# Kernel optimization log

Hardware: AMD Instinct MI355X
Metric: run time of the kernel (lower is better)

The kernel has to match this reference:

```python
import jax, jax.numpy as jnp
import numpy as np

SLOPE = 0.01

def leaky_tanh(x):
    return jnp.tanh(x * (2.0 / 3.0)) * 1.7159 + x * SLOPE

def lstm_cell(x, h, c, w_ih, w_hh, b_ih, b_hh):
    # torch LSTMCell gate order: i, f, g, o
    gates = x @ w_ih.T + b_ih + h @ w_hh.T + b_hh
    i, f, g, o = jnp.split(gates, 4, axis=-1)
    c_new = jax.nn.sigmoid(f) * c + jax.nn.sigmoid(i) * jnp.tanh(g)
    h_new = jax.nn.sigmoid(o) * jnp.tanh(c_new)
    return h_new, c_new

def setup_inputs() -> dict:
    key = jax.random.key(0)
    ks = jax.random.split(key, 16)
    T, B, I, H, O = 512, 64, 128, 2048, 64
    H1, H2 = H // 2, H // 8  # 1024, 256
    F2 = H // 4              # 512
    s = 0.02
    return {
        "inputs": jax.random.normal(ks[0], (T, B, I), dtype=jnp.float32),
        "fc1_w": jax.random.normal(ks[1], (H, I), dtype=jnp.float32) * s,
        "fc1_b": jax.random.normal(ks[2], (H,), dtype=jnp.float32) * s,
        "w_ih1": jax.random.normal(ks[3], (4 * H1, H), dtype=jnp.float32) * s,
        "w_hh1": jax.random.normal(ks[4], (4 * H1, H1), dtype=jnp.float32) * s,
        "b_ih1": jax.random.normal(ks[5], (4 * H1,), dtype=jnp.float32) * s,
        "b_hh1": jax.random.normal(ks[6], (4 * H1,), dtype=jnp.float32) * s,
        "fc2_w": jax.random.normal(ks[7], (F2, H1), dtype=jnp.float32) * s,
        "fc2_b": jax.random.normal(ks[8], (F2,), dtype=jnp.float32) * s,
        "w_ih2": jax.random.normal(ks[9], (4 * H2, F2), dtype=jnp.float32) * s,
        "w_hh2": jax.random.normal(ks[10], (4 * H2, H2), dtype=jnp.float32) * s,
        "b_ih2": jax.random.normal(ks[11], (4 * H2,), dtype=jnp.float32) * s,
        "b_hh2": jax.random.normal(ks[12], (4 * H2,), dtype=jnp.float32) * s,
        "fc3_w": jax.random.normal(ks[13], (O, H2), dtype=jnp.float32) * s,
        "fc3_b": jax.random.normal(ks[14], (O,), dtype=jnp.float32) * s,
    }

def reference(inputs, fc1_w, fc1_b, w_ih1, w_hh1, b_ih1, b_hh1,
              fc2_w, fc2_b, w_ih2, w_hh2, b_ih2, b_hh2, fc3_w, fc3_b):
    T, B, _ = inputs.shape
    H1 = w_hh1.shape[1]
    H2 = w_hh2.shape[1]
    h1 = jnp.zeros((B, H1), dtype=inputs.dtype)
    c1 = jnp.zeros((B, H1), dtype=inputs.dtype)
    h2 = jnp.zeros((B, H2), dtype=inputs.dtype)
    c2 = jnp.zeros((B, H2), dtype=inputs.dtype)

    def step(carry, xt):
        h1, c1, h2, c2 = carry
        x = leaky_tanh(xt @ fc1_w.T + fc1_b)
        h1, c1 = lstm_cell(x, h1, c1, w_ih1, w_hh1, b_ih1, b_hh1)
        x = leaky_tanh(h1 @ fc2_w.T + fc2_b)
        h2, c2 = lstm_cell(x, h2, c2, w_ih2, w_hh2, b_ih2, b_hh2)
        yhat = h2 @ fc3_w.T + fc3_b
        return (h1, c1, h2, c2), yhat

    _, outputs = jax.lax.scan(step, (h1, c1, h2, c2), inputs)
    return outputs  # [T, B, output_size]
```

## Files before the change

### kernel.cpp

```cpp
#include <hip/hip_runtime.h>
#include <hip/hip_bf16.h>

static constexpr int T_  = 512;
static constexpr int B_  = 64;
static constexpr int I_  = 128;
static constexpr int H_  = 2048;
static constexpr int H1_ = 1024;
static constexpr int F2_ = 512;
static constexpr int H2_ = 256;
static constexpr int O_  = 64;
static constexpr int G1N = 4096;
static constexpr int G2N = 1024;

typedef __attribute__((ext_vector_type(8))) __bf16 bfx8;
typedef __attribute__((ext_vector_type(4))) __bf16 bfx4;
typedef __attribute__((ext_vector_type(4))) float  fx4;

#define DEV __device__ __forceinline__

DEV fx4 mfma16(bfx8 a, bfx8 b, fx4 c) {
  return __builtin_amdgcn_mfma_f32_16x16x32_bf16(a, b, c, 0, 0, 0);
}
DEV float fast_sig(float x) { return 1.0f / (1.0f + __expf(-x)); }
DEV float fast_tanh(float x) {
  x = fminf(fmaxf(x, -30.0f), 30.0f);
  return 2.0f / (1.0f + __expf(-2.0f * x)) - 1.0f;
}
DEV float leaky_tanh_(float x) { return fast_tanh(x * (2.0f / 3.0f)) * 1.7159f + 0.01f * x; }

DEV void gld16c(const void* g, void* l) {
  __builtin_amdgcn_global_load_lds(
      (const __attribute__((address_space(1))) unsigned int*)g,
      (__attribute__((address_space(3))) unsigned int*)l, 16, 0, 17);
}
DEV void spin_ge(int* p, int tgt) {
  while (__hip_atomic_load(p, __ATOMIC_RELAXED, __HIP_MEMORY_SCOPE_AGENT) < tgt)
    __builtin_amdgcn_s_sleep(2);
}
DEV void stc2(unsigned short* p, unsigned short v) {
  __hip_atomic_store(p, v, __ATOMIC_RELAXED, __HIP_MEMORY_SCOPE_AGENT);
}
DEV unsigned long long ldc8(const void* p) {
  return __hip_atomic_load((const unsigned long long*)p, __ATOMIC_RELAXED,
                           __HIP_MEMORY_SCOPE_AGENT);
}
DEV unsigned short bf16bits(float f) {
  __bf16 h = (__bf16)f;
  return __builtin_bit_cast(unsigned short, h);
}

__global__ void k_f2b(const float* __restrict__ s, __bf16* __restrict__ d, int n4) {
  int i = blockIdx.x * blockDim.x + threadIdx.x;
  int st = gridDim.x * blockDim.x;
  for (; i < n4; i += st) {
    float4 v = ((const float4*)s)[i];
    bfx4 o = { (__bf16)v.x, (__bf16)v.y, (__bf16)v.z, (__bf16)v.w };
    ((bfx4*)d)[i] = o;
  }
}
__global__ void k_add2(const float* __restrict__ a, const float* __restrict__ b,
                       float* __restrict__ d, int n) {
  int i = blockIdx.x * blockDim.x + threadIdx.x;
  if (i < n) d[i] = a[i] + b[i];
}

__global__ void k_wre1(const float* __restrict__ w, __bf16* __restrict__ W2) {
  int v = blockIdx.x * 256 + threadIdx.x;
  int l = v & 63, kk = (v >> 6) & 31, g = (v >> 11) & 3, ng = v >> 13;
  int row = g * 1024 + ng * 16 + (l & 15);
  int k0  = kk * 32 + (l >> 4) * 8;
  const float* sp = w + (size_t)row * 1024 + k0;
  float4 v0 = ((const float4*)sp)[0];
  float4 v1 = ((const float4*)sp)[1];
  bfx8 o = { (__bf16)v0.x, (__bf16)v0.y, (__bf16)v0.z, (__bf16)v0.w,
             (__bf16)v1.x, (__bf16)v1.y, (__bf16)v1.z, (__bf16)v1.w };
  *(bfx8*)(W2 + (size_t)v * 8) = o;
}

__launch_bounds__(256)
__global__ void k_gemm(const __bf16* __restrict__ A, const __bf16* __restrict__ W,
                       __bf16* __restrict__ outB, const float* __restrict__ bias,
                       int M, int N, int K, int epi)
{
  __shared__ __bf16 As[128][32];
  __shared__ __bf16 Ws[128][32];
  const int tid = threadIdx.x;
  const int lane = tid & 63;
  const int wave = tid >> 6;
  const int wm = wave >> 1, wn = wave & 1;
  const int m0 = blockIdx.y * 128, n0 = blockIdx.x * 128;
  const int r1 = tid >> 2, c1v = (tid & 3) * 8;
  const int kr = (lane >> 4) * 8, rr = lane & 15;
  fx4 acc[4][4] = {};
  for (int k0 = 0; k0 < K; k0 += 32) {
    __syncthreads();
    *(bfx8*)&As[r1][c1v]      = *(const bfx8*)&A[(size_t)(m0 + r1) * K + k0 + c1v];
    *(bfx8*)&As[r1 + 64][c1v] = *(const bfx8*)&A[(size_t)(m0 + r1 + 64) * K + k0 + c1v];
    *(bfx8*)&Ws[r1][c1v]      = *(const bfx8*)&W[(size_t)(n0 + r1) * K + k0 + c1v];
    *(bfx8*)&Ws[r1 + 64][c1v] = *(const bfx8*)&W[(size_t)(n0 + r1 + 64) * K + k0 + c1v];
    __syncthreads();
    bfx8 a[4], b[4];
#pragma unroll
    for (int mi = 0; mi < 4; ++mi) a[mi] = *(const bfx8*)&As[wm*64 + mi*16 + rr][kr];
#pragma unroll
    for (int ni = 0; ni < 4; ++ni) b[ni] = *(const bfx8*)&Ws[wn*64 + ni*16 + rr][kr];
#pragma unroll
    for (int mi = 0; mi < 4; ++mi)
#pragma unroll
      for (int ni = 0; ni < 4; ++ni)
        acc[mi][ni] = mfma16(a[mi], b[ni], acc[mi][ni]);
  }
  const int cr = (lane >> 4) * 4, cc = lane & 15;
#pragma unroll
  for (int mi = 0; mi < 4; ++mi)
#pragma unroll
    for (int ni = 0; ni < 4; ++ni) {
      int col = n0 + wn*64 + ni*16 + cc;
#pragma unroll
      for (int r = 0; r < 4; ++r) {
        int row = m0 + wm*64 + mi*16 + cr + r;
        float v = acc[mi][ni][r] + bias[col];
        outB[(size_t)row * N + col] = (__bf16)(epi == 1 ? leaky_tanh_(v) : v);
      }
    }
}

DEV void stage(char* dst, int rsB, const __bf16* __restrict__ src, size_t sStride,
               int n, int lg) {
  for (int idx = threadIdx.x; idx < n; idx += 256) {
    int r = idx >> lg, c = idx & ((1 << lg) - 1);
    *(bfx8*)(dst + r * rsB + ((c * 16) ^ ((r & 7) << 4))) =
        *(const bfx8*)(src + (size_t)r * sStride + c * 8);
  }
}

__launch_bounds__(256, 1)
__global__ void k_persist2(const __bf16* __restrict__ W2,
                           const __bf16* __restrict__ whh2b,
                           const __bf16* __restrict__ G1cb, const __bf16* __restrict__ G2cb,
                           __bf16* __restrict__ h1c, float* __restrict__ c1,
                           __bf16* __restrict__ h2a, float* __restrict__ c2,
                           int* __restrict__ cnt,
                           int Tc, int s0slot, int t2base, int do_l1, int do_l2)
{
  __shared__ __align__(16) char smem[131072];
  const int tid = threadIdx.x, lane = tid & 63, wv = tid >> 6;
  const int rr = lane & 15, hi = lane >> 4;
  const int col = tid & 15, brow = tid >> 4;
  const int bid = blockIdx.x;
  const bool isL1 = do_l1 && (bid < 64);

  if (isL1) {
    const int ng = bid;
    char* As = smem;
    float* Cp = (float*)smem;

    bfx8 wreg[4][8];
#pragma unroll
    for (int g = 0; g < 4; ++g)
#pragma unroll
      for (int j = 0; j < 8; ++j)
        wreg[g][j] = *(const bfx8*)(W2 + (size_t)((ng * 4 + g) * 32 + wv * 8 + j) * 512 + lane * 8);

    float pc[4];
#pragma unroll
    for (int q = 0; q < 4; ++q)
      pc[q] = c1[(brow + q * 16) * 1024 + ng * 16 + col];

    for (int s = 0; s < Tc; ++s) {
      float pg[4][4];
#pragma unroll
      for (int q = 0; q < 4; ++q)
#pragma unroll
        for (int g = 0; g < 4; ++g)
          pg[q][g] = (float)G1cb[(size_t)(s * 64 + brow + q * 16) * 4096 + g * 1024 + ng * 16 + col];

      if (s > 0 && tid < 4) spin_ge(cnt + tid * 128, 16 * s);
      __syncthreads();

      const __bf16* h1s = h1c + (size_t)(s == 0 ? s0slot : s) * 65536;
      {
        char* dstb = smem + wv * 32768;
#pragma unroll 8
        for (int i = 0; i < 32; ++i) {
          int d = wv * 2048 + i * 64 + lane;
          int r = d >> 7;
          int sg = (r << 7) | ((d & 127) ^ (r & 7));
          gld16c(h1s + (size_t)sg * 8, dstb + i * 1024);
        }
      }
      __syncthreads();

      fx4 acc[4][4] = {};
#pragma unroll
      for (int j = 0; j < 8; ++j) {
        const int kB = (wv * 8 + j) * 64 + hi * 16;
        bfx8 a[4];
#pragma unroll
        for (int m = 0; m < 4; ++m) {
          int ra = m * 16 + rr;
          a[m] = *(const bfx8*)(As + ra * 2048 + (kB ^ ((ra & 7) << 4)));
        }
#pragma unroll
        for (int g = 0; g < 4; ++g)
#pragma unroll
          for (int m = 0; m < 4; ++m)
            acc[g][m] = mfma16(a[m], wreg[g][j], acc[g][m]);
      }
      __syncthreads();
#pragma unroll
      for (int g = 0; g < 4; ++g)
#pragma unroll
        for (int m = 0; m < 4; ++m) {
          int gc = g * 16 + rr;
          int bx = (m * 16 + hi * 4) ^ ((gc & 15) << 2);
          *(fx4*)(Cp + ((wv * 64 + gc) * 64 + bx)) = acc[g][m];
        }
      __syncthreads();

      __bf16* h1o = h1c + (size_t)(s + 1) * 65536;
#pragma unroll
      for (int q = 0; q < 4; ++q) {
        int b_ = brow + q * 16;
        float gv[4];
#pragma unroll
        for (int g = 0; g < 4; ++g) {
          int gc = g * 16 + col;
          int bx = b_ ^ ((gc & 15) << 2);
          float v = pg[q][g];
#pragma unroll
          for (int w = 0; w < 4; ++w)
            v += Cp[(w * 64 + gc) * 64 + bx];
          gv[g] = v;
        }
        float cn = fast_sig(gv[1]) * pc[q] + fast_sig(gv[0]) * fast_tanh(gv[2]);
        pc[q] = cn;
        float hv = fast_sig(gv[3]) * fast_tanh(cn);
        stc2((unsigned short*)h1o + (b_ * 1024 + ng * 16 + col), bf16bits(hv));
      }
      __syncthreads();
      if (tid == 0)
        __hip_atomic_fetch_add(cnt + (ng & 3) * 128, 1, __ATOMIC_RELAXED,
                               __HIP_MEMORY_SCOPE_AGENT);
    }
#pragma unroll
    for (int q = 0; q < 4; ++q)
      c1[(brow + q * 16) * 1024 + ng * 16 + col] = pc[q];
  } else {
    if (!do_l2) return;
    const int ng2 = do_l1 ? bid - 64 : bid;
    if (ng2 >= 16) return;
    char* Ws2 = smem;
    char* As2 = smem + 32768;
    float (*Gx2)[64][16] = (float (*)[64][16])(smem + 32768);

    for (int idx = tid; idx < 2048; idx += 256) {
      int r = idx >> 5, c = idx & 31;
      int wr = (r >> 4) * 256 + ng2 * 16 + (r & 15);
      *(bfx8*)(Ws2 + r * 512 + ((c * 16) ^ ((r & 7) << 4))) =
          *(const bfx8*)(whh2b + (size_t)wr * 256 + c * 8);
    }
    float pc2[4];
#pragma unroll
    for (int q = 0; q < 4; ++q)
      pc2[q] = c2[(brow + q * 16) * 256 + ng2 * 16 + col];
    __syncthreads();

    for (int s = 0; s < Tc; ++s) {
      float pg[4][4];
#pragma unroll
      for (int q = 0; q < 4; ++q)
#pragma unroll
        for (int g = 0; g < 4; ++g)
          pg[q][g] = (float)G2cb[(size_t)(s * 64 + brow + q * 16) * 1024 + g * 256 + ng2 * 16 + col];

      if (s > 0 && tid == 0) spin_ge(cnt + 512, 16 * s);
      __syncthreads();

      const __bf16* h2s = h2a + (size_t)(t2base + s) * 16384;
      for (int idx = tid; idx < 2048; idx += 256) {
        int r = idx >> 5, c = idx & 31;
        const char* sp = (const char*)(h2s + r * 256 + c * 8);
        unsigned long long lo = ldc8(sp), hi8 = ldc8(sp + 8);
        char* dp = As2 + r * 512 + ((c * 16) ^ ((r & 7) << 4));
        *(unsigned long long*)dp = lo;
        *(unsigned long long*)(dp + 8) = hi8;
      }
      __syncthreads();

      fx4 acc[4] = {};
#pragma unroll
      for (int ks = 0; ks < 8; ++ks) {
        const int cb = ks * 64 + hi * 16;
        int rb = wv * 16 + rr;
        bfx8 bfr = *(const bfx8*)(Ws2 + rb * 512 + (cb ^ ((rb & 7) << 4)));
#pragma unroll
        for (int m = 0; m < 4; ++m) {
          int ra = m * 16 + rr;
          bfx8 afr = *(const bfx8*)(As2 + ra * 512 + (cb ^ ((ra & 7) << 4)));
          acc[m] = mfma16(afr, bfr, acc[m]);
        }
      }
      __syncthreads();
#pragma unroll
      for (int m = 0; m < 4; ++m)
#pragma unroll
        for (int r = 0; r < 4; ++r)
          Gx2[wv][m * 16 + hi * 4 + r][rr] = acc[m][r];
      __syncthreads();

      __bf16* h2o = h2a + (size_t)(t2base + s + 1) * 16384;
#pragma unroll
      for (int q = 0; q < 4; ++q) {
        int b_ = brow + q * 16;
        float gi = Gx2[0][b_][col] + pg[q][0];
        float gf = Gx2[1][b_][col] + pg[q][1];
        float gg = Gx2[2][b_][col] + pg[q][2];
        float go = Gx2[3][b_][col] + pg[q][3];
        float cn = fast_sig(gf) * pc2[q] + fast_sig(gi) * fast_tanh(gg);
        pc2[q] = cn;
        float hv = fast_sig(go) * fast_tanh(cn);
        stc2((unsigned short*)h2o + (b_ * 256 + ng2 * 16 + col), bf16bits(hv));
      }
      __syncthreads();
      if (tid == 0)
        __hip_atomic_fetch_add(cnt + 512, 1, __ATOMIC_RELAXED,
                               __HIP_MEMORY_SCOPE_AGENT);
    }
#pragma unroll
    for (int q = 0; q < 4; ++q)
      c2[(brow + q * 16) * 256 + ng2 * 16 + col] = pc2[q];
  }
}

__launch_bounds__(256)
__global__ void k_fc3b(const __bf16* __restrict__ H2mat, const __bf16* __restrict__ w3,
                       const float* __restrict__ b3, float* __restrict__ out)
{
  __shared__ __align__(16) char smem[65536];
  const int tid = threadIdx.x, lane = tid & 63, wv = tid >> 6;
  const int rr = lane & 15, hi = lane >> 4;
  char* As = smem;
  char* Ws = smem + 32768;
  const size_t row0 = (size_t)blockIdx.x * 64;
  stage(As, 512, H2mat + row0 * 256, 256, 2048, 5);
  stage(Ws, 512, w3, 256, 2048, 5);
  __syncthreads();
  fx4 acc[4] = {};
#pragma unroll
  for (int ks = 0; ks < 8; ++ks) {
    const int cbB = ks * 64 + hi * 16;
    int rb = wv * 16 + rr;
    bfx8 bfr = *(const bfx8*)(Ws + rb * 512 + (cbB ^ ((rb & 7) << 4)));
#pragma unroll
    for (int m = 0; m < 4; ++m) {
      int ra = m * 16 + rr;
      bfx8 afr = *(const bfx8*)(As + ra * 512 + (cbB ^ ((ra & 7) << 4)));
      acc[m] = mfma16(afr, bfr, acc[m]);
    }
  }
  float bv = b3[wv * 16 + rr];
#pragma unroll
  for (int m = 0; m < 4; ++m)
#pragma unroll
    for (int r = 0; r < 4; ++r)
      out[(row0 + m * 16 + hi * 4 + r) * 64 + wv * 16 + rr] = acc[m][r] + bv;
}

extern "C" void kernel_launch(void* const* d_in, const int* in_sizes, int n_in,
                              void* d_out, int out_size, void* d_ws, size_t ws_size,
                              hipStream_t stream)
{
  (void)in_sizes; (void)n_in; (void)out_size;
  const float* f_in = (const float*)d_in[0];
  const float* fc1w = (const float*)d_in[1];
  const float* fc1b = (const float*)d_in[2];
  const float* wih1 = (const float*)d_in[3];
  const float* whh1 = (const float*)d_in[4];
  const float* bih1 = (const float*)d_in[5];
  const float* bhh1 = (const float*)d_in[6];
  const float* fc2w = (const float*)d_in[7];
  const float* fc2b = (const float*)d_in[8];
  const float* wih2 = (const float*)d_in[9];
  const float* whh2 = (const float*)d_in[10];
  const float* bih2 = (const float*)d_in[11];
  const float* bhh2 = (const float*)d_in[12];
  const float* fc3w = (const float*)d_in[13];
  const float* fc3b = (const float*)d_in[14];
  float* out = (float*)d_out;

  char* base = (char*)d_ws;
  size_t off = 0;
  auto alloc = [&](size_t bytes) -> char* {
    char* q = base + off;
    off = (off + bytes + 255) & ~(size_t)255;
    return q;
  };
  __bf16* wb_fc1 = (__bf16*)alloc((size_t)H_ * I_ * 2);
  __bf16* wb_ih1 = (__bf16*)alloc((size_t)G1N * H_ * 2);
  __bf16* W2     = (__bf16*)alloc((size_t)G1N * H1_ * 2);
  __bf16* wb_fc2 = (__bf16*)alloc((size_t)F2_ * H1_ * 2);
  __bf16* wb_ih2 = (__bf16*)alloc((size_t)G2N * F2_ * 2);
  __bf16* wb_hh2 = (__bf16*)alloc((size_t)G2N * H2_ * 2);
  __bf16* wb_fc3 = (__bf16*)alloc((size_t)O_ * H2_ * 2);
  __bf16* in_bf  = (__bf16*)alloc((size_t)T_ * B_ * I_ * 2);
  float*  bsum1  = (float*) alloc((size_t)G1N * 4);
  float*  bsum2  = (float*) alloc((size_t)G2N * 4);
  float*  c1     = (float*) alloc((size_t)B_ * H1_ * 4);
  float*  c2     = (float*) alloc((size_t)B_ * H2_ * 4);
  __bf16* h2a    = (__bf16*)alloc((size_t)(T_ + 1) * B_ * H2_ * 2);
  int*    cnt    = (int*)   alloc(4096);
  size_t fixed = off;

  auto perTc = [](size_t Tc) -> size_t {
    size_t Mc = Tc * 64;
    return Mc * H_ * 2 + Mc * G1N * 2 + (Tc + 1) * (size_t)B_ * H1_ * 2
         + Mc * F2_ * 2 + Mc * G2N * 2 + 6 * 256;
  };
  int Tc = 128;
  while (Tc > 2 && fixed + perTc(Tc) > ws_size) Tc >>= 1;
  const int Mc = Tc * 64;
  __bf16* Xc   = (__bf16*)alloc((size_t)Mc * H_ * 2);
  __bf16* G1cb = (__bf16*)alloc((size_t)Mc * G1N * 2);
  __bf16* h1c  = (__bf16*)alloc((size_t)(Tc + 1) * B_ * H1_ * 2);
  __bf16* x2c  = (__bf16*)alloc((size_t)Mc * F2_ * 2);
  __bf16* G2cb = (__bf16*)alloc((size_t)Mc * G2N * 2);

  struct CV { const float* s; __bf16* d; int n; } cvs[7] = {
    {fc1w, wb_fc1, H_ * I_},   {wih1, wb_ih1, G1N * H_},
    {fc2w, wb_fc2, F2_ * H1_}, {wih2, wb_ih2, G2N * F2_}, {whh2, wb_hh2, G2N * H2_},
    {fc3w, wb_fc3, O_ * H2_},  {f_in, in_bf, T_ * B_ * I_},
  };
  for (int i = 0; i < 7; ++i) {
    int n4 = cvs[i].n / 4;
    int blocks = (n4 + 255) / 256;
    if (blocks > 2048) blocks = 2048;
    k_f2b<<<blocks, 256, 0, stream>>>(cvs[i].s, cvs[i].d, n4);
  }
  k_wre1<<<2048, 256, 0, stream>>>(whh1, W2);
  k_add2<<<G1N / 256, 256, 0, stream>>>(bih1, bhh1, bsum1, G1N);
  k_add2<<<G2N / 256, 256, 0, stream>>>(bih2, bhh2, bsum2, G2N);
  hipMemsetAsync(c1, 0, (size_t)B_ * H1_ * 4, stream);
  hipMemsetAsync(c2, 0, (size_t)B_ * H2_ * 4, stream);
  hipMemsetAsync(h1c, 0, (size_t)B_ * H1_ * 2, stream);
  hipMemsetAsync(h2a, 0, (size_t)B_ * H2_ * 2, stream);

  const int chunks = T_ / Tc;
  for (int ch = 0; ch < chunks; ++ch) {
    k_gemm<<<dim3(H_ / 128, Mc / 128), 256, 0, stream>>>(
        in_bf + (size_t)ch * Mc * I_, wb_fc1, Xc, fc1b, Mc, H_, I_, 1);
    k_gemm<<<dim3(G1N / 128, Mc / 128), 256, 0, stream>>>(
        Xc, wb_ih1, G1cb, bsum1, Mc, G1N, H_, 3);
    hipMemsetAsync(cnt, 0, 4096, stream);
    int do_l2 = (int)(ch > 0);
    k_persist2<<<do_l2 ? 80 : 64, 256, 0, stream>>>(
        W2, wb_hh2, G1cb, G2cb, h1c, c1, h2a, c2, cnt,
        Tc, (ch == 0) ? 0 : Tc, (ch - 1) * Tc, 1, do_l2);
    k_gemm<<<dim3(F2_ / 128, Mc / 128), 256, 0, stream>>>(
        h1c + (size_t)B_ * H1_, wb_fc2, x2c, fc2b, Mc, F2_, H1_, 1);
    k_gemm<<<dim3(G2N / 128, Mc / 128), 256, 0, stream>>>(
        x2c, wb_ih2, G2cb, bsum2, Mc, G2N, F2_, 3);
  }
  hipMemsetAsync(cnt, 0, 4096, stream);
  k_persist2<<<16, 256, 0, stream>>>(
      W2, wb_hh2, G1cb, G2cb, h1c, c1, h2a, c2, cnt,
      Tc, 0, (chunks - 1) * Tc, 0, 1);
  k_fc3b<<<(T_ * B_) / 64, 256, 0, stream>>>(h2a + (size_t)B_ * H2_, wb_fc3, fc3b, out);
}
```

Before: 4.064 ms.

## Overlap chunk GEMMs with recurrent layers inside one persistent kernel

Folds the per-chunk fc1, ih1, fc2 and ih2 GEMMs into the persistent recurrent kernel. 176 extra workgroups compute the next chunks' input projections and the previous chunk's layer-2 inputs while the layer-1 and layer-2 recurrences run. Buffers are double-buffered, and layer 2 waits on an atomic counter until its G2 inputs are ready. This hides the serial GEMM launches behind the latency-bound recurrence, at the cost of competing for CUs and memory bandwidth and more workspace. The spin sleep is also shortened.

```diff
diff --git a/kernel.cpp b/kernel.cpp
--- a/kernel.cpp
+++ b/kernel.cpp
@@ -11,6 +11,7 @@
 static constexpr int O_  = 64;
 static constexpr int G1N = 4096;
 static constexpr int G2N = 1024;
+static constexpr int NW  = 176;
 
 typedef __attribute__((ext_vector_type(8))) __bf16 bfx8;
 typedef __attribute__((ext_vector_type(4))) __bf16 bfx4;
@@ -35,7 +36,7 @@
 }
 DEV void spin_ge(int* p, int tgt) {
   while (__hip_atomic_load(p, __ATOMIC_RELAXED, __HIP_MEMORY_SCOPE_AGENT) < tgt)
-    __builtin_amdgcn_s_sleep(2);
+    __builtin_amdgcn_s_sleep(1);
 }
 DEV void stc2(unsigned short* p, unsigned short v) {
   __hip_atomic_store(p, v, __ATOMIC_RELAXED, __HIP_MEMORY_SCOPE_AGENT);
@@ -47,6 +48,9 @@
 DEV unsigned short bf16bits(float f) {
   __bf16 h = (__bf16)f;
   return __builtin_bit_cast(unsigned short, h);
+}
+DEV void arrive1(int* p) {
+  __hip_atomic_fetch_add(p, 1, __ATOMIC_RELAXED, __HIP_MEMORY_SCOPE_AGENT);
 }
 
 __global__ void k_f2b(const float* __restrict__ s, __bf16* __restrict__ d, int n4) {
@@ -77,18 +81,14 @@
   *(bfx8*)(W2 + (size_t)v * 8) = o;
 }
 
-__launch_bounds__(256)
-__global__ void k_gemm(const __bf16* __restrict__ A, const __bf16* __restrict__ W,
-                       __bf16* __restrict__ outB, const float* __restrict__ bias,
-                       int M, int N, int K, int epi)
+DEV void gemm_tile(char* sm, const __bf16* __restrict__ A, const __bf16* __restrict__ W,
+                   __bf16* __restrict__ outB, const float* __restrict__ bias,
+                   int m0, int n0, int N, int K, int epi, int wt)
 {
-  __shared__ __bf16 As[128][32];
-  __shared__ __bf16 Ws[128][32];
-  const int tid = threadIdx.x;
-  const int lane = tid & 63;
-  const int wave = tid >> 6;
+  __bf16 (*As)[32] = (__bf16 (*)[32])sm;
+  __bf16 (*Ws)[32] = (__bf16 (*)[32])(sm + 8192);
+  const int tid = threadIdx.x, lane = tid & 63, wave = tid >> 6;
   const int wm = wave >> 1, wn = wave & 1;
-  const int m0 = blockIdx.y * 128, n0 = blockIdx.x * 128;
   const int r1 = tid >> 2, c1v = (tid & 3) * 8;
   const int kr = (lane >> 4) * 8, rr = lane & 15;
   fx4 acc[4][4] = {};
@@ -120,9 +120,21 @@
       for (int r = 0; r < 4; ++r) {
         int row = m0 + wm*64 + mi*16 + cr + r;
         float v = acc[mi][ni][r] + bias[col];
-        outB[(size_t)row * N + col] = (__bf16)(epi == 1 ? leaky_tanh_(v) : v);
-      }
-    }
+        if (epi == 1) v = leaky_tanh_(v);
+        if (wt) stc2((unsigned short*)outB + ((size_t)row * N + col), bf16bits(v));
+        else    outB[(size_t)row * N + col] = (__bf16)v;
+      }
+    }
+}
+
+__launch_bounds__(256)
+__global__ void k_gemm(const __bf16* __restrict__ A, const __bf16* __restrict__ W,
+                       __bf16* __restrict__ outB, const float* __restrict__ bias,
+                       int M, int N, int K, int epi)
+{
+  __shared__ __align__(16) char sm[16384];
+  (void)M;
+  gemm_tile(sm, A, W, outB, bias, blockIdx.y * 128, blockIdx.x * 128, N, K, epi, 0);
 }
 
 DEV void stage(char* dst, int rsB, const __bf16* __restrict__ src, size_t sStride,
@@ -134,23 +146,34 @@
   }
 }
 
+struct KP {
+  const __bf16 *W2, *whh2b;
+  const __bf16 *g1rd;  __bf16 *g1wr;
+  const __bf16 *xcrd;  __bf16 *xcwr;
+  const __bf16 *infc1;
+  const __bf16 *h1rd;  const __bf16 *h1s0;  __bf16 *h1wr;
+  __bf16 *x2c; __bf16 *g2;
+  const __bf16 *wfc1, *wih1, *wfc2, *wih2;
+  const float *bfc1, *bs1, *bfc2, *bs2;
+  float *c1, *c2;
+  __bf16 *h2a;
+  int *cnt;
+  int Tc, t2base, do_l1, do_l2, do_fc2, do_ih1, do_fc1;
+};
+
 __launch_bounds__(256, 1)
-__global__ void k_persist2(const __bf16* __restrict__ W2,
-                           const __bf16* __restrict__ whh2b,
-                           const __bf16* __restrict__ G1cb, const __bf16* __restrict__ G2cb,
-                           __bf16* __restrict__ h1c, float* __restrict__ c1,
-                           __bf16* __restrict__ h2a, float* __restrict__ c2,
-                           int* __restrict__ cnt,
-                           int Tc, int s0slot, int t2base, int do_l1, int do_l2)
+__global__ void k_persist3(KP p)
 {
   __shared__ __align__(16) char smem[131072];
   const int tid = threadIdx.x, lane = tid & 63, wv = tid >> 6;
   const int rr = lane & 15, hi = lane >> 4;
   const int col = tid & 15, brow = tid >> 4;
   const int bid = blockIdx.x;
-  const bool isL1 = do_l1 && (bid < 64);
-
-  if (isL1) {
+  int* cnt = p.cnt;
+  const int Tc = p.Tc;
+
+  if (bid < 64) {
+    if (!p.do_l1) return;
     const int ng = bid;
     char* As = smem;
     float* Cp = (float*)smem;
@@ -160,12 +183,12 @@
     for (int g = 0; g < 4; ++g)
 #pragma unroll
       for (int j = 0; j < 8; ++j)
-        wreg[g][j] = *(const bfx8*)(W2 + (size_t)((ng * 4 + g) * 32 + wv * 8 + j) * 512 + lane * 8);
+        wreg[g][j] = *(const bfx8*)(p.W2 + (size_t)((ng * 4 + g) * 32 + wv * 8 + j) * 512 + lane * 8);
 
     float pc[4];
 #pragma unroll
     for (int q = 0; q < 4; ++q)
-      pc[q] = c1[(brow + q * 16) * 1024 + ng * 16 + col];
+      pc[q] = p.c1[(brow + q * 16) * 1024 + ng * 16 + col];
 
     for (int s = 0; s < Tc; ++s) {
       float pg[4][4];
@@ -173,12 +196,12 @@
       for (int q = 0; q < 4; ++q)
 #pragma unroll
         for (int g = 0; g < 4; ++g)
-          pg[q][g] = (float)G1cb[(size_t)(s * 64 + brow + q * 16) * 4096 + g * 1024 + ng * 16 + col];
+          pg[q][g] = (float)p.g1rd[(size_t)(s * 64 + brow + q * 16) * 4096 + g * 1024 + ng * 16 + col];
 
       if (s > 0 && tid < 4) spin_ge(cnt + tid * 128, 16 * s);
       __syncthreads();
 
-      const __bf16* h1s = h1c + (size_t)(s == 0 ? s0slot : s) * 65536;
+      const __bf16* h1s = (s == 0) ? p.h1s0 : (p.h1wr + (size_t)s * 65536);
       {
         char* dstb = smem + wv * 32768;
 #pragma unroll 8
@@ -218,7 +241,7 @@
         }
       __syncthreads();
 
-      __bf16* h1o = h1c + (size_t)(s + 1) * 65536;
+      __bf16* h1o = p.h1wr + (size_t)(s + 1) * 65536;
 #pragma unroll
       for (int q = 0; q < 4; ++q) {
         int b_ = brow + q * 16;
@@ -239,17 +262,15 @@
         stc2((unsigned short*)h1o + (b_ * 1024 + ng * 16 + col), bf16bits(hv));
       }
       __syncthreads();
-      if (tid == 0)
-        __hip_atomic_fetch_add(cnt + (ng & 3) * 128, 1, __ATOMIC_RELAXED,
-                               __HIP_MEMORY_SCOPE_AGENT);
+      if (tid == 0) arrive1(cnt + (ng & 3) * 128);
     }
 #pragma unroll
     for (int q = 0; q < 4; ++q)
-      c1[(brow + q * 16) * 1024 + ng * 16 + col] = pc[q];
-  } else {
-    if (!do_l2) return;
-    const int ng2 = do_l1 ? bid - 64 : bid;
-    if (ng2 >= 16) return;
+      p.c1[(brow + q * 16) * 1024 + ng * 16 + col] = pc[q];
+
+  } else if (bid < 80) {
+    if (!p.do_l2) return;
+    const int ng2 = bid - 64;
     char* Ws2 = smem;
     char* As2 = smem + 32768;
     float (*Gx2)[64][16] = (float (*)[64][16])(smem + 32768);
@@ -258,12 +279,14 @@
       int r = idx >> 5, c = idx & 31;
       int wr = (r >> 4) * 256 + ng2 * 16 + (r & 15);
       *(bfx8*)(Ws2 + r * 512 + ((c * 16) ^ ((r & 7) << 4))) =
-          *(const bfx8*)(whh2b + (size_t)wr * 256 + c * 8);
+          *(const bfx8*)(p.whh2b + (size_t)wr * 256 + c * 8);
     }
     float pc2[4];
 #pragma unroll
     for (int q = 0; q < 4; ++q)
-      pc2[q] = c2[(brow + q * 16) * 256 + ng2 * 16 + col];
+      pc2[q] = p.c2[(brow + q * 16) * 256 + ng2 * 16 + col];
+
+    if (tid == 0) spin_ge(cnt + 640, NW);
     __syncthreads();
 
     for (int s = 0; s < Tc; ++s) {
@@ -272,12 +295,12 @@
       for (int q = 0; q < 4; ++q)
 #pragma unroll
         for (int g = 0; g < 4; ++g)
-          pg[q][g] = (float)G2cb[(size_t)(s * 64 + brow + q * 16) * 1024 + g * 256 + ng2 * 16 + col];
+          pg[q][g] = (float)p.g2[(size_t)(s * 64 + brow + q * 16) * 1024 + g * 256 + ng2 * 16 + col];
 
       if (s > 0 && tid == 0) spin_ge(cnt + 512, 16 * s);
       __syncthreads();
 
-      const __bf16* h2s = h2a + (size_t)(t2base + s) * 16384;
+      const __bf16* h2s = p.h2a + (size_t)(p.t2base + s) * 16384;
       for (int idx = tid; idx < 2048; idx += 256) {
         int r = idx >> 5, c = idx & 31;
         const char* sp = (const char*)(h2s + r * 256 + c * 8);
@@ -309,7 +332,7 @@
           Gx2[wv][m * 16 + hi * 4 + r][rr] = acc[m][r];
       __syncthreads();
 
-      __bf16* h2o = h2a + (size_t)(t2base + s + 1) * 16384;
+      __bf16* h2o = p.h2a + (size_t)(p.t2base + s + 1) * 16384;
 #pragma unroll
       for (int q = 0; q < 4; ++q) {
         int b_ = brow + q * 16;
@@ -323,13 +346,38 @@
         stc2((unsigned short*)h2o + (b_ * 256 + ng2 * 16 + col), bf16bits(hv));
       }
       __syncthreads();
-      if (tid == 0)
-        __hip_atomic_fetch_add(cnt + 512, 1, __ATOMIC_RELAXED,
-                               __HIP_MEMORY_SCOPE_AGENT);
+      if (tid == 0) arrive1(cnt + 512);
     }
 #pragma unroll
     for (int q = 0; q < 4; ++q)
-      c2[(brow + q * 16) * 256 + ng2 * 16 + col] = pc2[q];
+      p.c2[(brow + q * 16) * 256 + ng2 * 16 + col] = pc2[q];
+
+  } else {
+    const int wid = bid - 80;
+    const int Mt = (Tc * 64) / 128;
+    if (p.do_fc2) {
+      for (int i = wid; i < Mt * 4; i += NW)
+        gemm_tile(smem, p.h1rd + 65536, p.wfc2, p.x2c, p.bfc2,
+                  (i >> 2) * 128, (i & 3) * 128, F2_, H1_, 1, 1);
+      __syncthreads();
+      if (tid == 0) { arrive1(cnt + 576); spin_ge(cnt + 576, NW); }
+      __syncthreads();
+      for (int i = wid; i < Mt * 8; i += NW)
+        gemm_tile(smem, p.x2c, p.wih2, p.g2, p.bs2,
+                  (i >> 3) * 128, (i & 7) * 128, G2N, F2_, 0, 1);
+      __syncthreads();
+      if (tid == 0) arrive1(cnt + 640);
+    }
+    if (p.do_ih1) {
+      for (int i = wid; i < Mt * 32; i += NW)
+        gemm_tile(smem, p.xcrd, p.wih1, p.g1wr, p.bs1,
+                  (i >> 5) * 128, (i & 31) * 128, G1N, H_, 0, 0);
+    }
+    if (p.do_fc1) {
+      for (int i = wid; i < Mt * 16; i += NW)
+        gemm_tile(smem, p.infc1, p.wfc1, p.xcwr, p.bfc1,
+                  (i >> 4) * 128, (i & 15) * 128, H_, I_, 1, 0);
+    }
   }
 }
 
@@ -409,20 +457,28 @@
   float*  c1     = (float*) alloc((size_t)B_ * H1_ * 4);
   float*  c2     = (float*) alloc((size_t)B_ * H2_ * 4);
   __bf16* h2a    = (__bf16*)alloc((size_t)(T_ + 1) * B_ * H2_ * 2);
+  __bf16* h1zero = (__bf16*)alloc((size_t)B_ * H1_ * 2);
   int*    cnt    = (int*)   alloc(4096);
   size_t fixed = off;
 
   auto perTc = [](size_t Tc) -> size_t {
     size_t Mc = Tc * 64;
-    return Mc * H_ * 2 + Mc * G1N * 2 + (Tc + 1) * (size_t)B_ * H1_ * 2
-         + Mc * F2_ * 2 + Mc * G2N * 2 + 6 * 256;
+    return 2 * Mc * H_ * 2
+         + 2 * Mc * G1N * 2
+         + 2 * (Tc + 1) * (size_t)B_ * H1_ * 2
+         + Mc * F2_ * 2
+         + Mc * G2N * 2
+         + 10 * 256;
   };
   int Tc = 128;
   while (Tc > 2 && fixed + perTc(Tc) > ws_size) Tc >>= 1;
   const int Mc = Tc * 64;
-  __bf16* Xc   = (__bf16*)alloc((size_t)Mc * H_ * 2);
-  __bf16* G1cb = (__bf16*)alloc((size_t)Mc * G1N * 2);
-  __bf16* h1c  = (__bf16*)alloc((size_t)(Tc + 1) * B_ * H1_ * 2);
+  __bf16* XcA  = (__bf16*)alloc((size_t)Mc * H_ * 2);
+  __bf16* XcB  = (__bf16*)alloc((size_t)Mc * H_ * 2);
+  __bf16* G1A  = (__bf16*)alloc((size_t)Mc * G1N * 2);
+  __bf16* G1B  = (__bf16*)alloc((size_t)Mc * G1N * 2);
+  __bf16* h1rA = (__bf16*)alloc((size_t)(Tc + 1) * B_ * H1_ * 2);
+  __bf16* h1rB = (__bf16*)alloc((size_t)(Tc + 1) * B_ * H1_ * 2);
   __bf16* x2c  = (__bf16*)alloc((size_t)Mc * F2_ * 2);
   __bf16* G2cb = (__bf16*)alloc((size_t)Mc * G2N * 2);
 
@@ -442,28 +498,48 @@
   k_add2<<<G2N / 256, 256, 0, stream>>>(bih2, bhh2, bsum2, G2N);
   hipMemsetAsync(c1, 0, (size_t)B_ * H1_ * 4, stream);
   hipMemsetAsync(c2, 0, (size_t)B_ * H2_ * 4, stream);
-  hipMemsetAsync(h1c, 0, (size_t)B_ * H1_ * 2, stream);
+  hipMemsetAsync(h1zero, 0, (size_t)B_ * H1_ * 2, stream);
   hipMemsetAsync(h2a, 0, (size_t)B_ * H2_ * 2, stream);
 
   const int chunks = T_ / Tc;
-  for (int ch = 0; ch < chunks; ++ch) {
+  k_gemm<<<dim3(H_ / 128, Mc / 128), 256, 0, stream>>>(in_bf, wb_fc1, XcA, fc1b, Mc, H_, I_, 1);
+  k_gemm<<<dim3(G1N / 128, Mc / 128), 256, 0, stream>>>(XcA, wb_ih1, G1A, bsum1, Mc, G1N, H_, 0);
+  if (chunks > 1)
     k_gemm<<<dim3(H_ / 128, Mc / 128), 256, 0, stream>>>(
-        in_bf + (size_t)ch * Mc * I_, wb_fc1, Xc, fc1b, Mc, H_, I_, 1);
-    k_gemm<<<dim3(G1N / 128, Mc / 128), 256, 0, stream>>>(
-        Xc, wb_ih1, G1cb, bsum1, Mc, G1N, H_, 3);
+        in_bf + (size_t)Mc * I_, wb_fc1, XcB, fc1b, Mc, H_, I_, 1);
+
+  KP p;
+  p.W2 = W2; p.whh2b = wb_hh2;
+  p.wfc1 = wb_fc1; p.wih1 = wb_ih1; p.wfc2 = wb_fc2; p.wih2 = wb_ih2;
+  p.bfc1 = fc1b; p.bs1 = bsum1; p.bfc2 = fc2b; p.bs2 = bsum2;
+  p.c1 = c1; p.c2 = c2; p.h2a = h2a; p.cnt = cnt;
+  p.x2c = x2c; p.g2 = G2cb; p.Tc = Tc;
+
+  for (int k = 0; k < chunks; ++k) {
     hipMemsetAsync(cnt, 0, 4096, stream);
-    int do_l2 = (int)(ch > 0);
-    k_persist2<<<do_l2 ? 80 : 64, 256, 0, stream>>>(
-        W2, wb_hh2, G1cb, G2cb, h1c, c1, h2a, c2, cnt,
-        Tc, (ch == 0) ? 0 : Tc, (ch - 1) * Tc, 1, do_l2);
-    k_gemm<<<dim3(F2_ / 128, Mc / 128), 256, 0, stream>>>(
-        h1c + (size_t)B_ * H1_, wb_fc2, x2c, fc2b, Mc, F2_, H1_, 1);
-    k_gemm<<<dim3(G2N / 128, Mc / 128), 256, 0, stream>>>(
-        x2c, wb_ih2, G2cb, bsum2, Mc, G2N, F2_, 3);
+    p.g1rd = (k & 1) ? G1B : G1A;
+    p.g1wr = (k & 1) ? G1A : G1B;
+    p.xcrd = ((k + 1) & 1) ? XcB : XcA;
+    p.xcwr = (k & 1) ? XcB : XcA;
+    p.infc1 = (k + 2 < chunks) ? (in_bf + (size_t)(k + 2) * Mc * I_) : in_bf;
+    p.h1wr = (k & 1) ? h1rB : h1rA;
+    p.h1rd = (k & 1) ? h1rA : h1rB;
+    p.h1s0 = (k == 0) ? h1zero : (p.h1rd + (size_t)Tc * 65536);
+    p.t2base = (k - 1) * Tc;
+    p.do_l1 = 1;
+    p.do_l2 = (k >= 1);
+    p.do_fc2 = (k >= 1);
+    p.do_ih1 = (k + 1 < chunks);
+    p.do_fc1 = (k + 2 < chunks);
+    k_persist3<<<256, 256, 0, stream>>>(p);
   }
   hipMemsetAsync(cnt, 0, 4096, stream);
-  k_persist2<<<16, 256, 0, stream>>>(
-      W2, wb_hh2, G1cb, G2cb, h1c, c1, h2a, c2, cnt,
-      Tc, 0, (chunks - 1) * Tc, 0, 1);
+  p.h1rd = ((chunks - 1) & 1) ? h1rB : h1rA;
+  p.h1wr = p.h1rd == h1rA ? h1rB : h1rA;
+  p.h1s0 = h1zero;
+  p.g1rd = G1A; p.g1wr = G1B; p.xcrd = XcA; p.xcwr = XcB; p.infc1 = in_bf;
+  p.t2base = (chunks - 1) * Tc;
+  p.do_l1 = 0; p.do_l2 = 1; p.do_fc2 = 1; p.do_ih1 = 0; p.do_fc1 = 0;
+  k_persist3<<<256, 256, 0, stream>>>(p);
   k_fc3b<<<(T_ * B_) / 64, 256, 0, stream>>>(h2a + (size_t)B_ * H2_, wb_fc3, fc3b, out);
 }
```

Measured after the change: 3.445 ms. 1.18x faster.
